# Performance work log

Measured on AMD Instinct MI355X. Metric: run time of the kernel, lower is better.

Reference implementation:

```python
import jax, jax.numpy as jnp
import numpy as np

B, N_IN, N_OUT, K, V = 8, 2048, 2048, 64, 64


def setup_inputs() -> dict:
    key = jax.random.key(0)
    k1, k2, k3 = jax.random.split(key, 3)
    return {
        "key": jax.random.normal(k1, (B, N_IN, 1, K), dtype=jnp.float32),
        "query": jax.random.normal(k2, (B, 1, N_OUT, K), dtype=jnp.float32),
        "value": jax.random.normal(k3, (B, N_IN, V), dtype=jnp.float32),
    }


def reference(key, query, value):
    ks = key.shape[-1]
    # sum(key * query, 3) / sqrt(key_size)  ==  batched GEMM over key_size
    # weights: [B, n_inputs, n_outputs]
    weights = jnp.einsum("bik,bok->bio", key[:, :, 0, :], query[:, 0, :, :]) / jnp.sqrt(
        jnp.asarray(ks, dtype=key.dtype)
    )
    weights = jax.nn.softmax(weights, axis=1)  # softmax over n_inputs
    # sum(weights[...,None] * value[:,:,None,:], 1) -> [B, n_outputs, value_size]
    vals = jnp.einsum("bio,biv->bov", weights, value)
    # row-wise L2 normalize each [value_size] vector
    vals = vals / (jnp.linalg.norm(vals, axis=-1, keepdims=True) + 1e-12)
    values = jnp.swapaxes(vals, 1, 2)  # [B, value_size, n_outputs]
    return values, weights
```

## Files before the change

kernel.cpp:

```cpp
#include <hip/hip_runtime.h>

#define NB 8
#define NN 2048
#define KK 64
#define VV 64
#define SCALE 0.18033688011112043f

typedef __bf16 bfrag __attribute__((ext_vector_type(8)));
typedef float f32x4 __attribute__((ext_vector_type(4)));
typedef unsigned short u16x4 __attribute__((ext_vector_type(4)));
typedef unsigned short u16x8 __attribute__((ext_vector_type(8)));

__device__ __forceinline__ unsigned short bf16r(float f) {
  unsigned u = __float_as_uint(f);
  u += 0x7fffu + ((u >> 16) & 1u);
  return (unsigned short)(u >> 16);
}

__device__ __forceinline__ int swz(int row, int colByte) {
  return row * 128 + (colByte ^ ((row & 7) << 4));
}

__device__ __forceinline__ bfrag lds_frag(const unsigned short* base, int row, int colByte) {
  return *reinterpret_cast<const bfrag*>(reinterpret_cast<const char*>(base) + swz(row, colByte));
}

struct KS { float4 f[4]; };
__device__ __forceinline__ void k_load(KS& s, const float* __restrict__ g) {
  const float4* p = reinterpret_cast<const float4*>(g);
  s.f[0] = p[0]; s.f[1] = p[1]; s.f[2] = p[2]; s.f[3] = p[3];
}
__device__ __forceinline__ void k_write(const KS& s, unsigned short* lds, int row, int colByte) {
  const float* f = reinterpret_cast<const float*>(&s.f[0]);
  u16x8 a, b;
#pragma unroll
  for (int j = 0; j < 8; ++j) a[j] = bf16r(f[j]);
#pragma unroll
  for (int j = 0; j < 8; ++j) b[j] = bf16r(f[8 + j]);
  *reinterpret_cast<u16x8*>(reinterpret_cast<char*>(lds) + swz(row, colByte)) = a;
  *reinterpret_cast<u16x8*>(reinterpret_cast<char*>(lds) + swz(row, colByte + 16)) = b;
}

struct VS { float4 f[4]; };
__device__ __forceinline__ void v_load(VS& s, const float* __restrict__ g) {
  const float4* p = reinterpret_cast<const float4*>(g);
  s.f[0] = p[0]; s.f[1] = p[1];
  const float4* q = reinterpret_cast<const float4*>(g + VV);
  s.f[2] = q[0]; s.f[3] = q[1];
}
__device__ __forceinline__ void v_write(const VS& s, unsigned short* lds, int il, int v0) {
  const float* lo = reinterpret_cast<const float*>(&s.f[0]);
  const float* hi = reinterpret_cast<const float*>(&s.f[2]);
#pragma unroll
  for (int j = 0; j < 8; ++j) {
    unsigned pk = (unsigned)bf16r(lo[j]) | ((unsigned)bf16r(hi[j]) << 16);
    *reinterpret_cast<unsigned*>(reinterpret_cast<char*>(lds) + swz(v0 + j, il * 2)) = pk;
  }
}

#define CHUNK 512
#define IT 64
#define K1STEPS (CHUNK / IT)
#define SCR_STRIDE 4160

__global__ void __launch_bounds__(256) attn_pass1(
    const float* __restrict__ key, const float* __restrict__ query,
    const float* __restrict__ value, float* __restrict__ scratch)
{
  __shared__ __align__(16) unsigned short Kt[IT * KK];
  __shared__ __align__(16) unsigned short Vt[VV * IT];
  __shared__ __align__(16) unsigned short Qt[64 * KK];
  __shared__ __align__(16) unsigned short Et[64 * IT];
  __shared__ float Red[4][64];

  const int tid  = threadIdx.x;
  const int lane = tid & 63;
  const int wv   = tid >> 6;
  const int l15  = lane & 15;
  const int l4   = lane >> 4;

  const int b    = blockIdx.x & 7;
  const int rest = blockIdx.x >> 3;
  const int ot   = rest & 31;
  const int ci   = rest >> 5;
  const int o0   = ot * 64;
  const int ib0  = ci * CHUNK;

  const float* Kg = key   + (size_t)b * NN * KK;
  const float* Qg = query + (size_t)b * NN * KK;
  const float* Vg = value + (size_t)b * NN * VV;
  float* scr = scratch + (size_t)((b * 32 + ot) * 4 + ci) * SCR_STRIDE;

  const int krow = tid >> 2;
  const int kel  = (tid & 3) * 16;
  const int kcb  = (tid & 3) * 32;
  const int vil  = (tid & 31) * 2;
  const int vv0  = (tid >> 5) * 8;

  {
    KS qs;
    k_load(qs, Qg + (size_t)(o0 + krow) * KK + kel);
    k_write(qs, Qt, krow, kcb);
  }
  KS ks; VS vs;
  k_load(ks, Kg + (size_t)(ib0 + krow) * KK + kel);
  v_load(vs, Vg + (size_t)(ib0 + vil) * VV + vv0);
  k_write(ks, Kt, krow, kcb);
  v_write(vs, Vt, vil, vv0);
  __syncthreads();

  f32x4 uacc[4];
  float Dacc[4] = {0.f, 0.f, 0.f, 0.f};
#pragma unroll
  for (int s = 0; s < 4; ++s) { f32x4 z = {0.f, 0.f, 0.f, 0.f}; uacc[s] = z; }

  for (int t = 0; t < K1STEPS; ++t) {
    if (t + 1 < K1STEPS) {
      k_load(ks, Kg + (size_t)(ib0 + (t + 1) * IT + krow) * KK + kel);
      v_load(vs, Vg + (size_t)(ib0 + (t + 1) * IT + vil) * VV + vv0);
    }
    bfrag a0 = lds_frag(Kt, wv * 16 + l15, l4 * 16);
    bfrag a1 = lds_frag(Kt, wv * 16 + l15, 64 + l4 * 16);
#pragma unroll
    for (int s = 0; s < 4; ++s) {
      bfrag b0 = lds_frag(Qt, s * 16 + l15, l4 * 16);
      bfrag b1 = lds_frag(Qt, s * 16 + l15, 64 + l4 * 16);
      f32x4 z = {0.f, 0.f, 0.f, 0.f};
      z = __builtin_amdgcn_mfma_f32_16x16x32_bf16(a0, b0, z, 0, 0, 0);
      z = __builtin_amdgcn_mfma_f32_16x16x32_bf16(a1, b1, z, 0, 0, 0);
      f32x4 e;
#pragma unroll
      for (int r = 0; r < 4; ++r) e[r] = exp2f(z[r] * SCALE);
      Dacc[s] += e[0] + e[1] + e[2] + e[3];
      u16x4 pk;
#pragma unroll
      for (int r = 0; r < 4; ++r) pk[r] = bf16r(e[r]);
      *reinterpret_cast<u16x4*>(reinterpret_cast<char*>(Et) +
                                swz(s * 16 + l15, wv * 32 + l4 * 8)) = pk;
    }
    __syncthreads();
    if (t + 1 < K1STEPS) k_write(ks, Kt, krow, kcb);
    bfrag va0 = lds_frag(Vt, wv * 16 + l15, l4 * 16);
    bfrag va1 = lds_frag(Vt, wv * 16 + l15, 64 + l4 * 16);
#pragma unroll
    for (int s = 0; s < 4; ++s) {
      bfrag e0 = lds_frag(Et, s * 16 + l15, l4 * 16);
      bfrag e1 = lds_frag(Et, s * 16 + l15, 64 + l4 * 16);
      uacc[s] = __builtin_amdgcn_mfma_f32_16x16x32_bf16(va0, e0, uacc[s], 0, 0, 0);
      uacc[s] = __builtin_amdgcn_mfma_f32_16x16x32_bf16(va1, e1, uacc[s], 0, 0, 0);
    }
    __syncthreads();
    if (t + 1 < K1STEPS) v_write(vs, Vt, vil, vv0);
  }

#pragma unroll
  for (int s = 0; s < 4; ++s)
#pragma unroll
    for (int r = 0; r < 4; ++r)
      scr[(wv * 16 + l4 * 4 + r) * 64 + s * 16 + l15] = uacc[s][r];

#pragma unroll
  for (int s = 0; s < 4; ++s) {
    float d = Dacc[s];
    d += __shfl_xor(d, 16, 64);
    d += __shfl_xor(d, 32, 64);
    if (lane < 16) Red[wv][s * 16 + lane] = d;
  }
  __syncthreads();
  if (tid < 64)
    scr[4096 + tid] = Red[0][tid] + Red[1][tid] + Red[2][tid] + Red[3][tid];
}

__global__ void __launch_bounds__(256) attn_reduce(
    const float* __restrict__ scratch, float* __restrict__ outV,
    float* __restrict__ invD)
{
  __shared__ float R2[4][64];
  __shared__ float Nn[64];

  const int tid = threadIdx.x;
  const int b   = blockIdx.x & 7;
  const int ot  = blockIdx.x >> 3;
  const float* base = scratch + (size_t)(b * 32 + ot) * 4 * SCR_STRIDE;

  const int ol = tid & 63;
  const int vb = tid >> 6;

  float u[16];
#pragma unroll
  for (int j = 0; j < 16; ++j) u[j] = 0.f;
#pragma unroll
  for (int c = 0; c < 4; ++c) {
    const float* p = base + c * SCR_STRIDE;
#pragma unroll
    for (int j = 0; j < 16; ++j) u[j] += p[tid + j * 256];
  }
  float ssq = 0.f;
#pragma unroll
  for (int j = 0; j < 16; ++j) ssq += u[j] * u[j];
  R2[vb][ol] = ssq;
  __syncthreads();
  if (tid < 64) {
    float n = R2[0][tid] + R2[1][tid] + R2[2][tid] + R2[3][tid];
    Nn[tid] = 1.f / (sqrtf(n) + 1e-12f);
    float D = 0.f;
#pragma unroll
    for (int c = 0; c < 4; ++c) D += base[c * SCR_STRIDE + 4096 + tid];
    invD[b * NN + ot * 64 + tid] = 1.f / D;
  }
  __syncthreads();
  const float inn = Nn[ol];
  float* vp = outV + (size_t)b * VV * NN + ot * 64 + ol;
#pragma unroll
  for (int j = 0; j < 16; ++j)
    vp[(size_t)(vb + 4 * j) * NN] = u[j] * inn;
}

__global__ void __launch_bounds__(256) attn_weights(
    const float* __restrict__ key, const float* __restrict__ query,
    const float* __restrict__ invD, float* __restrict__ outWall)
{
  __shared__ __align__(16) unsigned short Kt2[128 * 64];
  __shared__ __align__(16) unsigned short Qt2[128 * 64];

  const int tid  = threadIdx.x;
  const int lane = tid & 63;
  const int wv   = tid >> 6;
  const int l15  = lane & 15;
  const int l4   = lane >> 4;

  const int b    = blockIdx.x & 7;
  const int rest = blockIdx.x >> 3;
  const int it   = rest & 15;
  const int ot   = rest >> 4;

  const float* Kg = key   + (size_t)b * NN * KK;
  const float* Qg = query + (size_t)b * NN * KK;
  float* outW = outWall + (size_t)b * NN * NN;

  const int krow = tid >> 2;
  const int kel  = (tid & 3) * 16;
  const int kcb  = (tid & 3) * 32;

  KS s0, s1, s2, s3;
  k_load(s0, Kg + (size_t)(it * 128 + krow) * KK + kel);
  k_load(s1, Kg + (size_t)(it * 128 + 64 + krow) * KK + kel);
  k_load(s2, Qg + (size_t)(ot * 128 + krow) * KK + kel);
  k_load(s3, Qg + (size_t)(ot * 128 + 64 + krow) * KK + kel);
  k_write(s0, Kt2, krow, kcb);
  k_write(s1, Kt2, krow + 64, kcb);
  k_write(s2, Qt2, krow, kcb);
  k_write(s3, Qt2, krow + 64, kcb);

  float invd[8];
#pragma unroll
  for (int s = 0; s < 8; ++s)
    invd[s] = invD[b * NN + ot * 128 + s * 16 + l15];
  __syncthreads();

  bfrag a0[2], a1[2];
#pragma unroll
  for (int m = 0; m < 2; ++m) {
    a0[m] = lds_frag(Kt2, wv * 32 + m * 16 + l15, l4 * 16);
    a1[m] = lds_frag(Kt2, wv * 32 + m * 16 + l15, 64 + l4 * 16);
  }
  f32x4 acc[2][8];
#pragma unroll
  for (int m = 0; m < 2; ++m)
#pragma unroll
    for (int s = 0; s < 8; ++s) { f32x4 z = {0.f, 0.f, 0.f, 0.f}; acc[m][s] = z; }

#pragma unroll
  for (int s = 0; s < 8; ++s) {
    bfrag b0 = lds_frag(Qt2, s * 16 + l15, l4 * 16);
    bfrag b1 = lds_frag(Qt2, s * 16 + l15, 64 + l4 * 16);
#pragma unroll
    for (int m = 0; m < 2; ++m) {
      acc[m][s] = __builtin_amdgcn_mfma_f32_16x16x32_bf16(a0[m], b0, acc[m][s], 0, 0, 0);
      acc[m][s] = __builtin_amdgcn_mfma_f32_16x16x32_bf16(a1[m], b1, acc[m][s], 0, 0, 0);
    }
  }

#pragma unroll
  for (int m = 0; m < 2; ++m)
#pragma unroll
    for (int s = 0; s < 8; ++s) {
      float* wp = outW + (size_t)(it * 128 + wv * 32 + m * 16 + l4 * 4) * NN +
                  ot * 128 + s * 16 + l15;
#pragma unroll
      for (int r = 0; r < 4; ++r)
        wp[(size_t)r * NN] = exp2f(acc[m][s][r] * SCALE) * invd[s];
    }
}

extern "C" void kernel_launch(void* const* d_in, const int* in_sizes, int n_in,
                              void* d_out, int out_size, void* d_ws, size_t ws_size,
                              hipStream_t stream) {
  (void)in_sizes; (void)n_in; (void)ws_size; (void)out_size;
  const float* key   = (const float*)d_in[0];
  const float* query = (const float*)d_in[1];
  const float* value = (const float*)d_in[2];
  float* out  = (float*)d_out;
  float* outV = out;
  float* outW = out + (size_t)NB * VV * NN;
  float* invD = (float*)d_ws;
  float* scratch = outW;

  attn_pass1 <<<dim3(NB * 32 * 4), dim3(256), 0, stream>>>(key, query, value, scratch);
  attn_reduce<<<dim3(NB * 32),     dim3(256), 0, stream>>>(scratch, outV, invD);
  attn_weights<<<dim3(NB * 16 * 16), dim3(256), 0, stream>>>(key, query, invD, outW);
}
```

Baseline: 70.97 us.

## Load Q fragments directly to registers and vectorize weight stores by swapping MFMA operands

In pass1 and the weights kernel, the query tile is no longer staged through LDS. Each lane loads its MFMA fragment straight from global memory and converts it to bf16 in registers. In the weights kernel the MFMA operands are swapped so each lane holds four consecutive output columns, which allows 16-byte vector stores of the large weights matrix instead of scalar strided stores, and invD is read as a float4. The reduce kernel now uses 512 threads per block with 8 value rows per thread. The changes cut LDS traffic and store instruction count, but the direct global fragment loads are less coalesced.

```diff
diff --git a/kernel.cpp b/kernel.cpp
--- a/kernel.cpp
+++ b/kernel.cpp
@@ -23,6 +23,15 @@
 
 __device__ __forceinline__ bfrag lds_frag(const unsigned short* base, int row, int colByte) {
   return *reinterpret_cast<const bfrag*>(reinterpret_cast<const char*>(base) + swz(row, colByte));
+}
+
+__device__ __forceinline__ bfrag g_frag(const float* __restrict__ g) {
+  const float4* p = reinterpret_cast<const float4*>(g);
+  float4 x = p[0], y = p[1];
+  u16x8 u;
+  u[0] = bf16r(x.x); u[1] = bf16r(x.y); u[2] = bf16r(x.z); u[3] = bf16r(x.w);
+  u[4] = bf16r(y.x); u[5] = bf16r(y.y); u[6] = bf16r(y.z); u[7] = bf16r(y.w);
+  union { u16x8 a; bfrag b; } c; c.a = u; return c.b;
 }
 
 struct KS { float4 f[4]; };
@@ -69,7 +78,6 @@
 {
   __shared__ __align__(16) unsigned short Kt[IT * KK];
   __shared__ __align__(16) unsigned short Vt[VV * IT];
-  __shared__ __align__(16) unsigned short Qt[64 * KK];
   __shared__ __align__(16) unsigned short Et[64 * IT];
   __shared__ float Red[4][64];
 
@@ -97,11 +105,14 @@
   const int vil  = (tid & 31) * 2;
   const int vv0  = (tid >> 5) * 8;
 
-  {
-    KS qs;
-    k_load(qs, Qg + (size_t)(o0 + krow) * KK + kel);
-    k_write(qs, Qt, krow, kcb);
-  }
+  bfrag qb0[4], qb1[4];
+#pragma unroll
+  for (int s = 0; s < 4; ++s) {
+    const float* qr = Qg + (size_t)(o0 + s * 16 + l15) * KK;
+    qb0[s] = g_frag(qr + l4 * 8);
+    qb1[s] = g_frag(qr + 32 + l4 * 8);
+  }
+
   KS ks; VS vs;
   k_load(ks, Kg + (size_t)(ib0 + krow) * KK + kel);
   v_load(vs, Vg + (size_t)(ib0 + vil) * VV + vv0);
@@ -123,11 +134,9 @@
     bfrag a1 = lds_frag(Kt, wv * 16 + l15, 64 + l4 * 16);
 #pragma unroll
     for (int s = 0; s < 4; ++s) {
-      bfrag b0 = lds_frag(Qt, s * 16 + l15, l4 * 16);
-      bfrag b1 = lds_frag(Qt, s * 16 + l15, 64 + l4 * 16);
       f32x4 z = {0.f, 0.f, 0.f, 0.f};
-      z = __builtin_amdgcn_mfma_f32_16x16x32_bf16(a0, b0, z, 0, 0, 0);
-      z = __builtin_amdgcn_mfma_f32_16x16x32_bf16(a1, b1, z, 0, 0, 0);
+      z = __builtin_amdgcn_mfma_f32_16x16x32_bf16(a0, qb0[s], z, 0, 0, 0);
+      z = __builtin_amdgcn_mfma_f32_16x16x32_bf16(a1, qb1[s], z, 0, 0, 0);
       f32x4 e;
 #pragma unroll
       for (int r = 0; r < 4; ++r) e[r] = exp2f(z[r] * SCALE);
@@ -171,11 +180,11 @@
     scr[4096 + tid] = Red[0][tid] + Red[1][tid] + Red[2][tid] + Red[3][tid];
 }
 
-__global__ void __launch_bounds__(256) attn_reduce(
+__global__ void __launch_bounds__(512) attn_reduce(
     const float* __restrict__ scratch, float* __restrict__ outV,
     float* __restrict__ invD)
 {
-  __shared__ float R2[4][64];
+  __shared__ float R2[8][64];
   __shared__ float Nn[64];
 
   const int tid = threadIdx.x;
@@ -184,24 +193,26 @@
   const float* base = scratch + (size_t)(b * 32 + ot) * 4 * SCR_STRIDE;
 
   const int ol = tid & 63;
-  const int vb = tid >> 6;
-
-  float u[16];
-#pragma unroll
-  for (int j = 0; j < 16; ++j) u[j] = 0.f;
+  const int vg = tid >> 6;
+
+  float u[8];
+#pragma unroll
+  for (int j = 0; j < 8; ++j) u[j] = 0.f;
 #pragma unroll
   for (int c = 0; c < 4; ++c) {
     const float* p = base + c * SCR_STRIDE;
 #pragma unroll
-    for (int j = 0; j < 16; ++j) u[j] += p[tid + j * 256];
+    for (int j = 0; j < 8; ++j) u[j] += p[(vg + 8 * j) * 64 + ol];
   }
   float ssq = 0.f;
 #pragma unroll
-  for (int j = 0; j < 16; ++j) ssq += u[j] * u[j];
-  R2[vb][ol] = ssq;
+  for (int j = 0; j < 8; ++j) ssq += u[j] * u[j];
+  R2[vg][ol] = ssq;
   __syncthreads();
   if (tid < 64) {
-    float n = R2[0][tid] + R2[1][tid] + R2[2][tid] + R2[3][tid];
+    float n = 0.f;
+#pragma unroll
+    for (int g = 0; g < 8; ++g) n += R2[g][tid];
     Nn[tid] = 1.f / (sqrtf(n) + 1e-12f);
     float D = 0.f;
 #pragma unroll
@@ -212,8 +223,8 @@
   const float inn = Nn[ol];
   float* vp = outV + (size_t)b * VV * NN + ot * 64 + ol;
 #pragma unroll
-  for (int j = 0; j < 16; ++j)
-    vp[(size_t)(vb + 4 * j) * NN] = u[j] * inn;
+  for (int j = 0; j < 8; ++j)
+    vp[(size_t)(vg + 8 * j) * NN] = u[j] * inn;
 }
 
 __global__ void __launch_bounds__(256) attn_weights(
@@ -221,7 +232,6 @@
     const float* __restrict__ invD, float* __restrict__ outWall)
 {
   __shared__ __align__(16) unsigned short Kt2[128 * 64];
-  __shared__ __align__(16) unsigned short Qt2[128 * 64];
 
   const int tid  = threadIdx.x;
   const int lane = tid & 63;
@@ -238,59 +248,47 @@
   const float* Qg = query + (size_t)b * NN * KK;
   float* outW = outWall + (size_t)b * NN * NN;
 
-  const int krow = tid >> 2;
-  const int kel  = (tid & 3) * 16;
-  const int kcb  = (tid & 3) * 32;
-
-  KS s0, s1, s2, s3;
-  k_load(s0, Kg + (size_t)(it * 128 + krow) * KK + kel);
-  k_load(s1, Kg + (size_t)(it * 128 + 64 + krow) * KK + kel);
-  k_load(s2, Qg + (size_t)(ot * 128 + krow) * KK + kel);
-  k_load(s3, Qg + (size_t)(ot * 128 + 64 + krow) * KK + kel);
-  k_write(s0, Kt2, krow, kcb);
-  k_write(s1, Kt2, krow + 64, kcb);
-  k_write(s2, Qt2, krow, kcb);
-  k_write(s3, Qt2, krow + 64, kcb);
-
-  float invd[8];
-#pragma unroll
-  for (int s = 0; s < 8; ++s)
-    invd[s] = invD[b * NN + ot * 128 + s * 16 + l15];
-  __syncthreads();
+  {
+    const int krow = tid >> 1;
+    const int half = (tid & 1);
+    KS sA, sB;
+    k_load(sA, Kg + (size_t)(it * 128 + krow) * KK + half * 32);
+    k_load(sB, Kg + (size_t)(it * 128 + krow) * KK + half * 32 + 16);
+    k_write(sA, Kt2, krow, half * 64);
+    k_write(sB, Kt2, krow, half * 64 + 32);
+  }
 
   bfrag a0[2], a1[2];
 #pragma unroll
   for (int m = 0; m < 2; ++m) {
-    a0[m] = lds_frag(Kt2, wv * 32 + m * 16 + l15, l4 * 16);
-    a1[m] = lds_frag(Kt2, wv * 32 + m * 16 + l15, 64 + l4 * 16);
-  }
-  f32x4 acc[2][8];
+    const float* qr = Qg + (size_t)(ot * 128 + wv * 32 + m * 16 + l15) * KK;
+    a0[m] = g_frag(qr + l4 * 8);
+    a1[m] = g_frag(qr + 32 + l4 * 8);
+  }
+  f32x4 id[2];
 #pragma unroll
   for (int m = 0; m < 2; ++m)
-#pragma unroll
-    for (int s = 0; s < 8; ++s) { f32x4 z = {0.f, 0.f, 0.f, 0.f}; acc[m][s] = z; }
+    id[m] = *reinterpret_cast<const f32x4*>(
+        &invD[b * NN + ot * 128 + wv * 32 + m * 16 + l4 * 4]);
+  __syncthreads();
 
 #pragma unroll
   for (int s = 0; s < 8; ++s) {
-    bfrag b0 = lds_frag(Qt2, s * 16 + l15, l4 * 16);
-    bfrag b1 = lds_frag(Qt2, s * 16 + l15, 64 + l4 * 16);
+    bfrag b0 = lds_frag(Kt2, s * 16 + l15, l4 * 16);
+    bfrag b1 = lds_frag(Kt2, s * 16 + l15, 64 + l4 * 16);
 #pragma unroll
     for (int m = 0; m < 2; ++m) {
-      acc[m][s] = __builtin_amdgcn_mfma_f32_16x16x32_bf16(a0[m], b0, acc[m][s], 0, 0, 0);
-      acc[m][s] = __builtin_amdgcn_mfma_f32_16x16x32_bf16(a1[m], b1, acc[m][s], 0, 0, 0);
+      f32x4 z = {0.f, 0.f, 0.f, 0.f};
+      z = __builtin_amdgcn_mfma_f32_16x16x32_bf16(a0[m], b0, z, 0, 0, 0);
+      z = __builtin_amdgcn_mfma_f32_16x16x32_bf16(a1[m], b1, z, 0, 0, 0);
+      f32x4 w;
+#pragma unroll
+      for (int r = 0; r < 4; ++r) w[r] = exp2f(z[r] * SCALE) * id[m][r];
+      float* wp = outW + (size_t)(it * 128 + s * 16 + l15) * NN +
+                  ot * 128 + wv * 32 + m * 16 + l4 * 4;
+      *reinterpret_cast<f32x4*>(wp) = w;
     }
   }
-
-#pragma unroll
-  for (int m = 0; m < 2; ++m)
-#pragma unroll
-    for (int s = 0; s < 8; ++s) {
-      float* wp = outW + (size_t)(it * 128 + wv * 32 + m * 16 + l4 * 4) * NN +
-                  ot * 128 + s * 16 + l15;
-#pragma unroll
-      for (int r = 0; r < 4; ++r)
-        wp[(size_t)r * NN] = exp2f(acc[m][s][r] * SCALE) * invd[s];
-    }
 }
 
 extern "C" void kernel_launch(void* const* d_in, const int* in_sizes, int n_in,
@@ -307,6 +305,6 @@
   float* scratch = outW;
 
   attn_pass1 <<<dim3(NB * 32 * 4), dim3(256), 0, stream>>>(key, query, value, scratch);
-  attn_reduce<<<dim3(NB * 32),     dim3(256), 0, stream>>>(scratch, outV, invD);
+  attn_reduce<<<dim3(NB * 32),     dim3(512), 0, stream>>>(scratch, outV, invD);
   attn_weights<<<dim3(NB * 16 * 16), dim3(256), 0, stream>>>(key, query, invD, outW);
 }
```

New measurement: 76.35 us. 7.6% more time.
